# Performance work log

Measured on AMD Instinct MI355X. Metric: run time of the kernel, lower is better.

Reference implementation:

```python
import jax, jax.numpy as jnp
import numpy as np

B, T, I, H, O = 128, 512, 512, 2048, 512

def setup_inputs() -> dict:
    key = jax.random.key(0)
    ks = jax.random.split(key, 10)
    s = lambda fan_in: 1.0 / np.sqrt(fan_in)
    return {
        "x": jax.random.normal(ks[0], (B, T, I), dtype=jnp.float32),
        "dt": jnp.zeros((1,), dtype=jnp.float32),            # torch init: Tensor([0])
        "a": jnp.ones((1,), dtype=jnp.float32),              # torch init: Tensor([1])
        "enc_w": jax.random.uniform(ks[1], (H, I), jnp.float32, -s(I), s(I)),
        "enc_b": jax.random.uniform(ks[2], (H,), jnp.float32, -s(I), s(I)),
        "rec_w": jax.random.uniform(ks[3], (H, H), jnp.float32, -s(H), s(H)),
        "rec_b": jax.random.uniform(ks[4], (H,), jnp.float32, -s(H), s(H)),
        "dec_w": jax.random.uniform(ks[5], (O, H), jnp.float32, -s(H), s(H)),
        "dec_b": jax.random.uniform(ks[6], (O,), jnp.float32, -s(H), s(H)),
        "hi_w": jax.random.uniform(ks[7], (H, 1), jnp.float32, -1.0, 1.0),
        "hi_b": jax.random.uniform(ks[8], (H,), jnp.float32, -1.0, 1.0),
    }

def reference(x, dt, a, enc_w, enc_b, rec_w, rec_b, dec_w, dec_b, hi_w, hi_b):
    # x: [B, T, I] -> time-major [T, B, I]
    xt = jnp.transpose(x, (1, 0, 2))
    sdt = jax.nn.sigmoid(dt[0])          # scalar gate
    av = a[0]
    # hidden_init(ones(B,1)) = hi_w[:,0] + hi_b, broadcast over batch
    h0 = jnp.broadcast_to(hi_w[:, 0] + hi_b, (x.shape[0], hi_b.shape[0]))
    # precompute encoder projection for all timesteps: [T, B, H]
    enc = jnp.einsum('tbi,hi->tbh', xt, enc_w) + enc_b

    def step(h, e_t):
        h = (1.0 - sdt) * h + sdt * jnp.tanh(e_t + av * (h @ rec_w.T + rec_b))
        y = h @ dec_w.T + dec_b
        return h, y

    hidden, output = jax.lax.scan(step, h0, enc)
    return output, hidden
```

## Files before the change

kernel.cpp:

```cpp
#include <hip/hip_runtime.h>
#include <hip/hip_bf16.h>
#include <cmath>

#define Bb 128
#define Tt 512
#define Ii 512
#define Hh 2048
#define Oo 512
#define REC_GRID 256

typedef __bf16 bf16_t;
typedef __bf16 bf16x8 __attribute__((ext_vector_type(8)));
typedef __bf16 bf16x4 __attribute__((ext_vector_type(4)));
typedef float  f32x4_t __attribute__((ext_vector_type(4)));
typedef unsigned long long u64;
typedef unsigned u32;

static __device__ __forceinline__ bf16_t to_b(float v){ return (bf16_t)v; }
static __device__ __forceinline__ float  b2f(unsigned short u){ unsigned x = ((unsigned)u)<<16; return __builtin_bit_cast(float, x); }
static __device__ __forceinline__ unsigned short f2bbits(float v){ return __builtin_bit_cast(unsigned short, to_b(v)); }

static __device__ __forceinline__ void gl_lds16(const void* g, void* l){
  __builtin_amdgcn_global_load_lds((const __attribute__((address_space(1))) void*)g,
                                   (__attribute__((address_space(3))) void*)l, 16, 0, 0);
}

#define REP16(M) M(0)M(1)M(2)M(3)M(4)M(5)M(6)M(7)M(8)M(9)M(10)M(11)M(12)M(13)M(14)M(15)

__global__ __launch_bounds__(256) void k_f2b(bf16_t* __restrict__ dst, const float* __restrict__ src){
  size_t i = ((size_t)blockIdx.x*256 + threadIdx.x)*4;
  float4 v = *(const float4*)(src + i);
  bf16x4 o; o[0]=to_b(v.x); o[1]=to_b(v.y); o[2]=to_b(v.z); o[3]=to_b(v.w);
  *(bf16x4*)(dst + i) = o;
}

__global__ __launch_bounds__(256) void k_init_h0(const float* __restrict__ hi_w, const float* __restrict__ hi_b,
                                                 bf16_t* __restrict__ h0b){
  int i = blockIdx.x*256 + threadIdx.x;
  bf16_t vb = to_b(hi_w[i] + hi_b[i]);
  for (int b=0;b<Bb;++b) h0b[(size_t)b*Hh + i] = vb;
}

__global__ __launch_bounds__(256) void k_convert_x(const float* __restrict__ x, bf16_t* __restrict__ x_tm){
  size_t idx = ((size_t)blockIdx.x*256 + threadIdx.x)*8;
  int    i0  = (int)(idx % Ii);
  size_t m   = idx / Ii;
  int    t   = (int)(m / Bb), b = (int)(m % Bb);
  const float* s = x + ((size_t)b*Tt + t)*Ii + i0;
  float4 v0 = *(const float4*)s, v1 = *(const float4*)(s+4);
  bf16x8 o;
  o[0]=to_b(v0.x); o[1]=to_b(v0.y); o[2]=to_b(v0.z); o[3]=to_b(v0.w);
  o[4]=to_b(v1.x); o[5]=to_b(v1.y); o[6]=to_b(v1.z); o[7]=to_b(v1.w);
  *(bf16x8*)(x_tm + idx) = o;
}

template<int ROWS, int KB>
static __device__ __forceinline__ void stage(const bf16_t* __restrict__ g, long ld, long row0, int k0,
                                             char* __restrict__ ldsT){
  constexpr int SLOTS = KB/8;
  constexpr int PT    = ROWS*SLOTS/256;
  #pragma unroll
  for (int j=0;j<PT;++j){
    int c    = threadIdx.x + 256*j;
    int row  = c / SLOTS, slot = c % SLOTS;
    uint4 v  = *(const uint4*)(g + (row0+row)*ld + k0 + slot*8);
    *(uint4*)(ldsT + row*(KB*2) + ((slot*16) ^ ((row&7)<<4))) = v;
  }
}

template<int KB>
static __device__ __forceinline__ bf16x8 frag(const char* __restrict__ ldsT, int row, int kk, int lane){
  int kbyte = kk*64 + ((lane>>4)<<4);
  return *(const bf16x8*)(ldsT + row*(KB*2) + (kbyte ^ ((row&7)<<4)));
}

template<int EPI>
__global__ __launch_bounds__(256) void gemm128(const bf16_t* __restrict__ A, long lda,
                                               const bf16_t* __restrict__ Bw, long ldb,
                                               const float* __restrict__ bias,
                                               void* __restrict__ Cout, long ldc, int K){
  constexpr int TM=128, TN=128, KB=64;
  __shared__ char lds[(TM+TN)*KB*2];
  char* ldsA = lds;
  char* ldsB = lds + TM*KB*2;
  long m0 = (long)blockIdx.x * TM;
  long n0 = (long)blockIdx.y * TN;
  int w = threadIdx.x >> 6, lane = threadIdx.x & 63;
  int wm = w >> 1, wn = w & 1;
  f32x4_t acc[4][4] = {};
  for (int k0=0;k0<K;k0+=KB){
    __syncthreads();
    stage<TM,KB>(A,  lda, m0, k0, ldsA);
    stage<TN,KB>(Bw, ldb, n0, k0, ldsB);
    __syncthreads();
    #pragma unroll
    for (int kk=0;kk<KB/32;++kk){
      bf16x8 af[4], bfv[4];
      #pragma unroll
      for (int f=0;f<4;++f){ int r = wm*64 + f*16 + (lane&15); af[f]  = frag<KB>(ldsA, r, kk, lane); }
      #pragma unroll
      for (int f=0;f<4;++f){ int r = wn*64 + f*16 + (lane&15); bfv[f] = frag<KB>(ldsB, r, kk, lane); }
      #pragma unroll
      for (int i=0;i<4;++i)
        #pragma unroll
        for (int j=0;j<4;++j)
          acc[i][j] = __builtin_amdgcn_mfma_f32_16x16x32_bf16(af[i], bfv[j], acc[i][j], 0,0,0);
    }
  }
  #pragma unroll
  for (int i=0;i<4;++i)
    #pragma unroll
    for (int j=0;j<4;++j)
      #pragma unroll
      for (int e=0;e<4;++e){
        long row = m0 + wm*64 + i*16 + ((lane>>4)<<2) + e;
        long col = n0 + wn*64 + j*16 + (lane&15);
        float v = acc[i][j][e] + bias[col];
        if (EPI==0) ((bf16_t*)Cout)[row*ldc + col] = to_b(v);
        else        ((float*) Cout)[row*ldc + col] = v;
      }
}

__global__ __launch_bounds__(512, 1) void rec_persist(
    const bf16_t* __restrict__ h0b, const bf16_t* __restrict__ W,
    bf16_t* __restrict__ EH, float* __restrict__ hfinal,
    const float* __restrict__ rec_b, const float* __restrict__ hi_w, const float* __restrict__ hi_b,
    const float* __restrict__ dtp, const float* __restrict__ ap,
    unsigned* __restrict__ cnt)
{
  __shared__ char lds[131072 + 16384 + 2048];
  char* Wb   = lds;
  char* hbuf = lds;
  char* red  = lds + 131072;
  u32*  xb   = (u32*)(lds + 131072 + 16384);

  const int bid = blockIdx.x;
  const int g   = bid & 3;
  const int n   = bid >> 2;
  const int m0  = g * 32;
  const int n0  = n * 32;
  unsigned* gcnt = cnt + g*512;
  const int tid = threadIdx.x, w = tid >> 6, lane = tid & 63;
  const int l15 = lane & 15, ks16 = (lane >> 4) << 4;
  const int ch = w & 1, kq = w >> 1;

  for (int it = 0; it < 16; ++it){
    int cid = it*512 + tid;
    int lc  = cid & 63, j = (cid >> 6) & 63, c = cid >> 12;
    uint4 v = *(const uint4*)(W + (size_t)(n0 + c*16 + (lc&15))*Hh + j*32 + ((lc>>4)<<3));
    *(uint4*)(Wb + (size_t)cid*16) = v;
  }
  __syncthreads();
  const char* wfb = Wb + ((size_t)(ch*64 + kq*16)*64 + lane)*16;
  #define WDECL(i) bf16x8 w##i = *(const bf16x8*)(wfb + (i)*1024);
  REP16(WDECL)
  #undef WDECL
  __syncthreads();

  const float s  = 1.f/(1.f + __expf(-dtp[0]));
  const float av = ap[0];
  const int   bh_o = w & 1, ch_o = (w >> 1) & 1, eh = w >> 2;
  const int   batch = m0 + bh_o*16 + l15;
  const int   hcol0 = n0 + ch_o*16 + ((lane >> 4) << 2) + eh*2;
  const int   lslot = (bh_o*16 + l15)*16 + ch_o*8 + (lane>>4)*2 + eh;
  float rb[2], hm[2];
  #pragma unroll
  for (int e=0;e<2;++e){ rb[e] = rec_b[hcol0+e]; hm[e] = hi_w[hcol0+e] + hi_b[hcol0+e]; }

  const int   axor = (l15 & 7) << 4;
  const char* hb0  = hbuf + kq*32768 + (size_t)l15*512;
  const char* hb1  = hb0 + 8192;
  const int   srow  = lane >> 5;
  const int   scolx = (lane & 31) << 4;
  const int co_b = m0 + (tid >> 4);
  const int co_c = n0 + (tid & 15)*2;

  for (int t = 0; t < Tt; ++t){
    const bf16_t* Asrc = (t==0) ? h0b : (EH + (size_t)(t-1)*(Bb*Hh));
    bf16_t* EHt = EH + (size_t)t*(Bb*Hh);

    u32 ecv = __hip_atomic_load((const u32*)(EHt + (size_t)co_b*Hh + co_c),
                                __ATOMIC_RELAXED, __HIP_MEMORY_SCOPE_AGENT);

    {
      char* dst = hbuf + w*16384;
      const char* asb = (const char*)Asrc + ((size_t)(m0 + srow))*(Hh*2) + w*512;
      #pragma unroll
      for (int i = 0; i < 16; ++i){
        int row = 2*i + srow;
        int cb  = scolx ^ ((row & 7) << 4);
        gl_lds16(asb + (size_t)(2*i)*(Hh*2) + cb, dst + (i<<10));
      }
    }
    __syncthreads();

    f32x4_t acc0 = {0.f,0.f,0.f,0.f}, acc1 = acc0;
    #define KSTEP(kk) { \
      int off = ((kk)>>3)*16384 + ((((kk)&7)*64 + ks16) ^ axor); \
      bf16x8 h0v = *(const bf16x8*)(hb0 + off); \
      acc0 = __builtin_amdgcn_mfma_f32_16x16x32_bf16(w##kk, h0v, acc0, 0,0,0); \
      bf16x8 h1v = *(const bf16x8*)(hb1 + off); \
      acc1 = __builtin_amdgcn_mfma_f32_16x16x32_bf16(w##kk, h1v, acc1, 0,0,0); }
    REP16(KSTEP)
    #undef KSTEP

    __syncthreads();
    *(f32x4_t*)(red + (((0*2 + ch)*4 + kq)*64 + lane)*16) = acc0;
    *(f32x4_t*)(red + (((1*2 + ch)*4 + kq)*64 + lane)*16) = acc1;
    xb[tid] = ecv;
    __syncthreads();
    const int rbase = ((bh_o*2 + ch_o)*4)*64 + lane;
    f32x4_t fa = *(const f32x4_t*)(red + rbase*16);
    #pragma unroll
    for (int q=1;q<4;++q) fa = fa + *(const f32x4_t*)(red + (rbase + q*64)*16);

    u32 ev = xb[lslot];
    u32 ov = 0;
    #pragma unroll
    for (int e=0;e<2;++e){
      float enc = b2f((unsigned short)(ev >> (16*e)));
      float pre = enc + av*(fa[eh*2+e] + rb[e]);
      float th  = 1.f - 2.f/(__expf(2.f*pre) + 1.f);
      hm[e] = (1.f - s)*hm[e] + s*th;
      ov |= ((u32)f2bbits(hm[e])) << (16*e);
    }
    xb[lslot] = ov;
    __syncthreads();
    u32 hv = xb[tid];
    __hip_atomic_store((u32*)(EHt + (size_t)co_b*Hh + co_c), hv,
                       __ATOMIC_RELAXED, __HIP_MEMORY_SCOPE_AGENT);
    __syncthreads();

    if (tid == 0){
      __hip_atomic_fetch_add(gcnt + t, 1u, __ATOMIC_RELAXED, __HIP_MEMORY_SCOPE_AGENT);
      while (__hip_atomic_load(gcnt + t, __ATOMIC_RELAXED, __HIP_MEMORY_SCOPE_AGENT) < 64u) {}
    }
    __syncthreads();
  }

  #pragma unroll
  for (int e=0;e<2;++e) hfinal[(size_t)batch*Hh + hcol0 + e] = hm[e];
}

extern "C" void kernel_launch(void* const* d_in, const int* in_sizes, int n_in,
                              void* d_out, int out_size, void* d_ws, size_t ws_size,
                              hipStream_t stream){
  const float* x     = (const float*)d_in[0];
  const float* dt    = (const float*)d_in[1];
  const float* a     = (const float*)d_in[2];
  const float* enc_w = (const float*)d_in[3];
  const float* enc_b = (const float*)d_in[4];
  const float* rec_w = (const float*)d_in[5];
  const float* rec_b = (const float*)d_in[6];
  const float* dec_w = (const float*)d_in[7];
  const float* dec_b = (const float*)d_in[8];
  const float* hi_w  = (const float*)d_in[9];
  const float* hi_b  = (const float*)d_in[10];
  float* out = (float*)d_out;

  char* ws = (char*)d_ws;
  size_t off = 0;
  auto carve = [&](size_t bytes)->char*{ char* p = ws + off; off += (bytes + 255) & ~(size_t)255; return p; };
  bf16_t* x_tm   = (bf16_t*)carve((size_t)Tt*Bb*Ii*2);
  bf16_t* EH     = (bf16_t*)carve((size_t)Tt*Bb*Hh*2);
  bf16_t* h0b    = (bf16_t*)carve((size_t)Bb*Hh*2);
  bf16_t* enc_wb = (bf16_t*)carve((size_t)Hh*Ii*2);
  bf16_t* rec_wb = (bf16_t*)carve((size_t)Hh*Hh*2);
  bf16_t* dec_wb = (bf16_t*)carve((size_t)Oo*Hh*2);
  unsigned* cnt  = (unsigned*)carve(4*512*4);
  if (off > ws_size) return;

  hipMemsetAsync(cnt, 0, 4*512*4, stream);

  k_f2b<<<(Hh*Ii)/1024, 256, 0, stream>>>(enc_wb, enc_w);
  k_f2b<<<(Hh*Hh)/1024, 256, 0, stream>>>(rec_wb, rec_w);
  k_f2b<<<(Oo*Hh)/1024, 256, 0, stream>>>(dec_wb, dec_w);
  k_init_h0<<<Hh/256, 256, 0, stream>>>(hi_w, hi_b, h0b);
  k_convert_x<<<((size_t)Tt*Bb*Ii/8)/256, 256, 0, stream>>>(x, x_tm);

  gemm128<0><<<dim3((Tt*Bb)/128, Hh/128), 256, 0, stream>>>(x_tm, Ii, enc_wb, Ii, enc_b, EH, Hh, Ii);

  {
    float* hfinal = out + (size_t)Tt*Bb*Oo;
    void* args[] = { (void*)&h0b, (void*)&rec_wb, (void*)&EH, (void*)&hfinal,
                     (void*)&rec_b, (void*)&hi_w, (void*)&hi_b, (void*)&dt, (void*)&a,
                     (void*)&cnt };
    hipLaunchCooperativeKernel((const void*)rec_persist, dim3(REC_GRID), dim3(512), args, 0, stream);
  }

  gemm128<1><<<dim3((Tt*Bb)/128, Oo/128), 256, 0, stream>>>(EH, Hh, dec_wb, Hh, dec_b, out, Oo, Hh);
}
```

Measured before the change: 2.854 ms.

## Retile persistent recurrence to 16 batch rows by 64 hidden columns per block

The persistent recurrent kernel now splits the 256 blocks into 8 batch groups of 16 rows and 32 column tiles of 64 hidden units, where it used 4 groups of 32 rows and 64 tiles of 32 columns. Each block keeps 64 columns of register-resident weights, loaded in two LDS passes, and applies four MFMA streams to each shared h fragment. This halves the per-step h tile each block loads and makes each grid-barrier group 32 blocks instead of 64. The cost is more weight registers, an 8-way instead of 4-way cross-wave reduction, and twice the weight bytes per block.

```diff
diff --git a/kernel.cpp b/kernel.cpp
--- a/kernel.cpp
+++ b/kernel.cpp
@@ -25,7 +25,7 @@
                                    (__attribute__((address_space(3))) void*)l, 16, 0, 0);
 }
 
-#define REP16(M) M(0)M(1)M(2)M(3)M(4)M(5)M(6)M(7)M(8)M(9)M(10)M(11)M(12)M(13)M(14)M(15)
+#define REP8(M) M(0)M(1)M(2)M(3)M(4)M(5)M(6)M(7)
 
 __global__ __launch_bounds__(256) void k_f2b(bf16_t* __restrict__ dst, const float* __restrict__ src){
   size_t i = ((size_t)blockIdx.x*256 + threadIdx.x)*4;
@@ -128,52 +128,62 @@
     const float* __restrict__ dtp, const float* __restrict__ ap,
     unsigned* __restrict__ cnt)
 {
-  __shared__ char lds[131072 + 16384 + 2048];
-  char* Wb   = lds;
+  __shared__ char lds[131072];
   char* hbuf = lds;
-  char* red  = lds + 131072;
-  u32*  xb   = (u32*)(lds + 131072 + 16384);
+  char* red  = lds + 65536;
+  u32*  xb   = (u32*)(lds + 65536 + 32768);
 
   const int bid = blockIdx.x;
-  const int g   = bid & 3;
-  const int n   = bid >> 2;
-  const int m0  = g * 32;
-  const int n0  = n * 32;
+  const int g   = bid & 7;
+  const int n   = bid >> 3;
+  const int m0  = g * 16;
+  const int n0  = n * 64;
   unsigned* gcnt = cnt + g*512;
   const int tid = threadIdx.x, w = tid >> 6, lane = tid & 63;
-  const int l15 = lane & 15, ks16 = (lane >> 4) << 4;
-  const int ch = w & 1, kq = w >> 1;
-
-  for (int it = 0; it < 16; ++it){
-    int cid = it*512 + tid;
-    int lc  = cid & 63, j = (cid >> 6) & 63, c = cid >> 12;
-    uint4 v = *(const uint4*)(W + (size_t)(n0 + c*16 + (lc&15))*Hh + j*32 + ((lc>>4)<<3));
-    *(uint4*)(Wb + (size_t)cid*16) = v;
-  }
-  __syncthreads();
-  const char* wfb = Wb + ((size_t)(ch*64 + kq*16)*64 + lane)*16;
-  #define WDECL(i) bf16x8 w##i = *(const bf16x8*)(wfb + (i)*1024);
-  REP16(WDECL)
-  #undef WDECL
+  const int l15 = lane & 15, w8 = w*8;
+
+  #define WDCL(i) bf16x8 wa##i, wb##i, wc##i, wd##i;
+  REP8(WDCL)
+  #undef WDCL
+  #pragma unroll 1
+  for (int p = 0; p < 2; ++p){
+    __syncthreads();
+    for (int it = 0; it < 16; ++it){
+      int cid = it*512 + tid;
+      int lc  = cid & 63, kk = (cid >> 6) & 63, cgl = cid >> 12;
+      uint4 v = *(const uint4*)(W + (size_t)(n0 + p*32 + cgl*16 + (lc&15))*Hh + kk*32 + ((lc>>4)<<3));
+      *(uint4*)(lds + (size_t)cid*16) = v;
+    }
+    __syncthreads();
+    if (p == 0){
+      #define WRD0(i) \
+        wa##i = *(const bf16x8*)(lds + (size_t)((      w8 + (i))*64 + lane)*16); \
+        wb##i = *(const bf16x8*)(lds + (size_t)((4096/64*0 + 64 + w8 + (i))*64 + lane)*16);
+      REP8(WRD0)
+      #undef WRD0
+    } else {
+      #define WRD1(i) \
+        wc##i = *(const bf16x8*)(lds + (size_t)((      w8 + (i))*64 + lane)*16); \
+        wd##i = *(const bf16x8*)(lds + (size_t)((64 + w8 + (i))*64 + lane)*16);
+      REP8(WRD1)
+      #undef WRD1
+    }
+  }
   __syncthreads();
 
   const float s  = 1.f/(1.f + __expf(-dtp[0]));
   const float av = ap[0];
-  const int   bh_o = w & 1, ch_o = (w >> 1) & 1, eh = w >> 2;
-  const int   batch = m0 + bh_o*16 + l15;
-  const int   hcol0 = n0 + ch_o*16 + ((lane >> 4) << 2) + eh*2;
-  const int   lslot = (bh_o*16 + l15)*16 + ch_o*8 + (lane>>4)*2 + eh;
+  const int   cg_o = w & 3, eh = w >> 2;
+  const int   batch = m0 + l15;
+  const int   hcol0 = n0 + cg_o*16 + ((lane>>4)<<2) + eh*2;
+  const int   lslot = l15*32 + cg_o*8 + (lane>>4)*2 + eh;
   float rb[2], hm[2];
   #pragma unroll
   for (int e=0;e<2;++e){ rb[e] = rec_b[hcol0+e]; hm[e] = hi_w[hcol0+e] + hi_b[hcol0+e]; }
 
-  const int   axor = (l15 & 7) << 4;
-  const char* hb0  = hbuf + kq*32768 + (size_t)l15*512;
-  const char* hb1  = hb0 + 8192;
-  const int   srow  = lane >> 5;
-  const int   scolx = (lane & 31) << 4;
-  const int co_b = m0 + (tid >> 4);
-  const int co_c = n0 + (tid & 15)*2;
+  const size_t vsrc_off = (size_t)(m0 + l15)*Hh + ((lane>>4)<<3);
+  const int co_b = m0 + (tid >> 5);
+  const int co_c = n0 + (tid & 31)*2;
 
   for (int t = 0; t < Tt; ++t){
     const bf16_t* Asrc = (t==0) ? h0b : (EH + (size_t)(t-1)*(Bb*Hh));
@@ -183,36 +193,32 @@
                                 __ATOMIC_RELAXED, __HIP_MEMORY_SCOPE_AGENT);
 
     {
-      char* dst = hbuf + w*16384;
-      const char* asb = (const char*)Asrc + ((size_t)(m0 + srow))*(Hh*2) + w*512;
-      #pragma unroll
-      for (int i = 0; i < 16; ++i){
-        int row = 2*i + srow;
-        int cb  = scolx ^ ((row & 7) << 4);
-        gl_lds16(asb + (size_t)(2*i)*(Hh*2) + cb, dst + (i<<10));
-      }
-    }
-    __syncthreads();
-
-    f32x4_t acc0 = {0.f,0.f,0.f,0.f}, acc1 = acc0;
-    #define KSTEP(kk) { \
-      int off = ((kk)>>3)*16384 + ((((kk)&7)*64 + ks16) ^ axor); \
-      bf16x8 h0v = *(const bf16x8*)(hb0 + off); \
-      acc0 = __builtin_amdgcn_mfma_f32_16x16x32_bf16(w##kk, h0v, acc0, 0,0,0); \
-      bf16x8 h1v = *(const bf16x8*)(hb1 + off); \
-      acc1 = __builtin_amdgcn_mfma_f32_16x16x32_bf16(w##kk, h1v, acc1, 0,0,0); }
-    REP16(KSTEP)
-    #undef KSTEP
-
-    __syncthreads();
-    *(f32x4_t*)(red + (((0*2 + ch)*4 + kq)*64 + lane)*16) = acc0;
-    *(f32x4_t*)(red + (((1*2 + ch)*4 + kq)*64 + lane)*16) = acc1;
+      const bf16_t* src = Asrc + vsrc_off;
+      #pragma unroll
+      for (int i = 0; i < 8; ++i)
+        gl_lds16(src + (w8 + i)*32, hbuf + (size_t)(w8 + i)*1024);
+    }
+    __syncthreads();
+
+    f32x4_t acc0 = {0.f,0.f,0.f,0.f}, acc1 = acc0, acc2 = acc0, acc3 = acc0;
+    #define KS(i) { \
+      bf16x8 hv = *(const bf16x8*)(hbuf + (size_t)(w8 + (i))*1024 + (size_t)lane*16); \
+      acc0 = __builtin_amdgcn_mfma_f32_16x16x32_bf16(wa##i, hv, acc0, 0,0,0); \
+      acc1 = __builtin_amdgcn_mfma_f32_16x16x32_bf16(wb##i, hv, acc1, 0,0,0); \
+      acc2 = __builtin_amdgcn_mfma_f32_16x16x32_bf16(wc##i, hv, acc2, 0,0,0); \
+      acc3 = __builtin_amdgcn_mfma_f32_16x16x32_bf16(wd##i, hv, acc3, 0,0,0); }
+    REP8(KS)
+    #undef KS
+
+    *(f32x4_t*)(red + (size_t)((w*4 + 0)*64 + lane)*16) = acc0;
+    *(f32x4_t*)(red + (size_t)((w*4 + 1)*64 + lane)*16) = acc1;
+    *(f32x4_t*)(red + (size_t)((w*4 + 2)*64 + lane)*16) = acc2;
+    *(f32x4_t*)(red + (size_t)((w*4 + 3)*64 + lane)*16) = acc3;
     xb[tid] = ecv;
     __syncthreads();
-    const int rbase = ((bh_o*2 + ch_o)*4)*64 + lane;
-    f32x4_t fa = *(const f32x4_t*)(red + rbase*16);
-    #pragma unroll
-    for (int q=1;q<4;++q) fa = fa + *(const f32x4_t*)(red + (rbase + q*64)*16);
+    f32x4_t fa = *(const f32x4_t*)(red + (size_t)((0*4 + cg_o)*64 + lane)*16);
+    #pragma unroll
+    for (int q=1;q<8;++q) fa = fa + *(const f32x4_t*)(red + (size_t)((q*4 + cg_o)*64 + lane)*16);
 
     u32 ev = xb[lslot];
     u32 ov = 0;
@@ -233,7 +239,7 @@
 
     if (tid == 0){
       __hip_atomic_fetch_add(gcnt + t, 1u, __ATOMIC_RELAXED, __HIP_MEMORY_SCOPE_AGENT);
-      while (__hip_atomic_load(gcnt + t, __ATOMIC_RELAXED, __HIP_MEMORY_SCOPE_AGENT) < 64u) {}
+      while (__hip_atomic_load(gcnt + t, __ATOMIC_RELAXED, __HIP_MEMORY_SCOPE_AGENT) < 32u) {}
     }
     __syncthreads();
   }
@@ -267,10 +273,10 @@
   bf16_t* enc_wb = (bf16_t*)carve((size_t)Hh*Ii*2);
   bf16_t* rec_wb = (bf16_t*)carve((size_t)Hh*Hh*2);
   bf16_t* dec_wb = (bf16_t*)carve((size_t)Oo*Hh*2);
-  unsigned* cnt  = (unsigned*)carve(4*512*4);
+  unsigned* cnt  = (unsigned*)carve(8*512*4);
   if (off > ws_size) return;
 
-  hipMemsetAsync(cnt, 0, 4*512*4, stream);
+  hipMemsetAsync(cnt, 0, 8*512*4, stream);
 
   k_f2b<<<(Hh*Ii)/1024, 256, 0, stream>>>(enc_wb, enc_w);
   k_f2b<<<(Hh*Hh)/1024, 256, 0, stream>>>(rec_wb, rec_w);
```

After: 2.886 ms. No clear change (+1.1%).
